# Performance work log

Hardware: AMD Instinct MI355X
Metric: run time of the kernel (lower is better)

Reference implementation:

```python
import jax, jax.numpy as jnp
import numpy as np

B, S, E, H = 4, 2048, 1024, 16
Dh = E // H
EPS = 1e-5


def setup_inputs() -> dict:
    key = jax.random.key(0)
    ks = jax.random.split(key, 16)
    w = lambda k, shp: jax.random.normal(k, shp, dtype=jnp.float32) * 0.02
    return {
        "x": jax.random.normal(ks[0], (B, S, E), dtype=jnp.float32),
        "Wq": w(ks[1], (E, E)), "bq": jnp.zeros((E,), jnp.float32),
        "Wk": w(ks[2], (E, E)), "bk": jnp.zeros((E,), jnp.float32),
        "Wv": w(ks[3], (E, E)), "bv": jnp.zeros((E,), jnp.float32),
        "Wo": w(ks[4], (E, E)), "bo": jnp.zeros((E,), jnp.float32),
        "an1_a": jnp.ones((1, S, 1), jnp.float32),
        "an1_b": jnp.zeros((1, S, 1), jnp.float32),
        "W1": w(ks[5], (2 * E, E)), "b1": jnp.zeros((2 * E,), jnp.float32),
        "W2": w(ks[6], (E, 2 * E)), "b2": jnp.zeros((E,), jnp.float32),
        "an2_a": jnp.ones((1, S, 1), jnp.float32),
        "an2_b": jnp.zeros((1, S, 1), jnp.float32),
    }


def adaptive_norm(x, a, b):
    # AdaptiveNorm((1, N_s, 1)): normalize over embedding dim, per-position affine.
    mu = jnp.mean(x, axis=-1, keepdims=True)
    var = jnp.mean(jnp.square(x - mu), axis=-1, keepdims=True)
    return a * (x - mu) * jax.lax.rsqrt(var + EPS) + b


def reference(x, Wq, bq, Wk, bk, Wv, bv, Wo, bo, an1_a, an1_b, W1, b1, W2, b2, an2_a, an2_b):
    scale = 1.0 / np.sqrt(E / H)
    # QKV projections -> (B, S, H, Dh)
    q = (x @ Wq.T + bq).reshape(B, S, H, Dh)
    k = (x @ Wk.T + bk).reshape(B, S, H, Dh)
    v = (x @ Wv.T + bv).reshape(B, S, H, Dh)
    # scaled dot-product attention (materializes B,H,S,S like the original)
    scores = jnp.einsum("bshd,bthd->bhst", q, k) * scale
    probs = jax.nn.softmax(scores, axis=-1)
    attn = jnp.einsum("bhst,bthd->bshd", probs, v).reshape(B, S, E)
    attn = attn @ Wo.T + bo
    # residual + adaptive norm (dropout is identity in eval mode)
    h = adaptive_norm(attn + x, an1_a, an1_b)
    ff = jax.nn.relu(h @ W1.T + b1) @ W2.T + b2
    out = adaptive_norm(ff + h, an2_a, an2_b)
    return out
```

## Files before the change

### kernel.cpp

```cpp
#include <hip/hip_runtime.h>


typedef __attribute__((ext_vector_type(8))) short s16x8;
typedef __attribute__((ext_vector_type(4))) short s16x4;
typedef __attribute__((ext_vector_type(4))) unsigned short u16x4;
typedef __attribute__((ext_vector_type(4))) float f32x4;

__device__ __forceinline__ float bf2f(unsigned short u) {
  unsigned int v = ((unsigned int)u) << 16;
  return __builtin_bit_cast(float, v);
}
__device__ __forceinline__ unsigned short f2bf(float f) {
  unsigned int u = __builtin_bit_cast(unsigned int, f);
  u += 0x7fffu + ((u >> 16) & 1u);
  return (unsigned short)(u >> 16);
}
__device__ __forceinline__ unsigned int pkbf_trunc(float f0, float f1) {
  return __builtin_amdgcn_perm(__builtin_bit_cast(unsigned int, f1),
                               __builtin_bit_cast(unsigned int, f0), 0x07060302u);
}
__device__ __forceinline__ f32x4 mfma16(s16x8 a, s16x8 b, f32x4 c) {
  return __builtin_amdgcn_mfma_f32_16x16x32_bf16(a, b, c, 0, 0, 0);
}
__device__ __forceinline__ void gl2lds16(const unsigned short* g, unsigned short* l) {
  __builtin_amdgcn_global_load_lds(
      (const __attribute__((address_space(1))) unsigned int*)(g),
      (__attribute__((address_space(3))) unsigned int*)(l), 16, 0, 0);
}

__global__ void detect_dtype(const unsigned int* __restrict__ x, int* __restrict__ flag) {
  const int tid = threadIdx.x;
  int cnt = 0;
  for (int i = tid; i < 2048; i += 256) {
    const unsigned e = (x[i] >> 7) & 0xFF;
    cnt += (e >= 100 && e <= 150) ? 1 : 0;
  }
#pragma unroll
  for (int off = 32; off >= 1; off >>= 1) cnt += __shfl_xor(cnt, off);
  __shared__ int red[4];
  if ((tid & 63) == 0) red[tid >> 6] = cnt;
  __syncthreads();
  if (tid == 0) *flag = ((red[0] + red[1] + red[2] + red[3]) > 1536) ? 1 : 0;
}

struct CvtArgs {
  const void* src[17];
  unsigned short* dst[17];
  int cum4[18];
};

__global__ __launch_bounds__(256) void cvt_all(CvtArgs a, const int* __restrict__ flag, int total4) {
  const int i = blockIdx.x * 256 + threadIdx.x;
  if (i >= total4) return;
  int lo = 0, hi = 17;
  while (hi - lo > 1) {
    const int mid = (lo + hi) >> 1;
    if (i >= a.cum4[mid]) lo = mid; else hi = mid;
  }
  const int off4 = i - a.cum4[lo];
  if (*flag) {
    const u16x4* s = (const u16x4*)a.src[lo];
    *(u16x4*)&a.dst[lo][off4 * 4] = s[off4];
  } else {
    const float4* s = (const float4*)a.src[lo];
    const float4 v = s[off4];
    u16x4 o;
    o[0] = f2bf(v.x); o[1] = f2bf(v.y); o[2] = f2bf(v.z); o[3] = f2bf(v.w);
    *(u16x4*)&a.dst[lo][off4 * 4] = o;
  }
}

#define QOFF 8388608L
#define SCALE2 0.18033688011f

template <int EPI, int BM>
__global__ __launch_bounds__(512, 1) void gemm2(
    const unsigned short* __restrict__ A, const unsigned short* __restrict__ W,
    const unsigned short* __restrict__ bias, const unsigned short* __restrict__ resid,
    unsigned short* __restrict__ out, int M, int N, int K) {
  constexpr int NBUF = (BM == 256) ? 2 : 3;
  constexpr int BUFE = (BM + 256) * 64;
  extern __shared__ unsigned short sh[];

  const int tid = threadIdx.x;
  const int lane = tid & 63;
  const int wave = tid >> 6;
  const int qd = lane >> 4;
  const int c = lane & 15;
  const int wr = (wave >> 2) * (BM / 2);
  const int wc = (wave & 3) * 64;

  const int nx = gridDim.x, ny = gridDim.y;
  const int nwg = nx * ny;
  int lin = blockIdx.y * nx + blockIdx.x;
  lin = (lin & 7) * (nwg >> 3) + (lin >> 3);
  const int by = lin % ny;
  const int bx = lin / ny;
  const long m0 = (long)by * BM;
  const long n0 = (long)bx * 256;

  const int srow = tid >> 3;
  const int scc = ((tid & 7) ^ (srow & 7)) * 8;
  const unsigned short* Asrc = A + (m0 + srow) * (long)K + scc;
  const unsigned short* Wsrc = W + (n0 + srow) * (long)K + scc;
  const int lofs = tid * 8;

  f32x4 acc[BM / 32][4] = {};

  const int NT = K >> 6;

  auto stA = [&](int sel, int tt, int q) {
    gl2lds16(Asrc + (long)q * 64 * K + (long)tt * 64, sh + sel * BUFE + q * 4096 + lofs);
  };
  auto stB = [&](int sel, int tt, int q) {
    gl2lds16(Wsrc + (long)q * 64 * K + (long)tt * 64,
             sh + sel * BUFE + BM * 64 + q * 4096 + lofs);
  };

  if constexpr (BM == 256) {
    stB(0, 0, 0); stB(0, 0, 1); stB(0, 0, 2); stB(0, 0, 3);
    stA(0, 0, 0); stA(0, 0, 2); stA(0, 0, 1); stA(0, 0, 3);
  } else {
    stB(0, 0, 0); stB(0, 0, 1); stB(0, 0, 2); stB(0, 0, 3); stA(0, 0, 0); stA(0, 0, 1);
    stB(1, 1, 0); stB(1, 1, 1); stB(1, 1, 2); stB(1, 1, 3); stA(1, 1, 0); stA(1, 1, 1);
  }

  int cur = 0;
  for (int t = 0; t < NT; ++t) {
    const unsigned short* Ab = sh + cur * BUFE;
    const unsigned short* Bb = Ab + BM * 64;

    if constexpr (BM == 256) {
      const bool dost = (t + 1 < NT);
      const int ns = cur ^ 1;
      asm volatile("s_waitcnt vmcnt(2)\n\ts_barrier" ::: "memory");
      s16x8 bfr[4][2], af[4][2];
#pragma unroll
      for (int nt = 0; nt < 4; ++nt)
#pragma unroll
        for (int ks = 0; ks < 2; ++ks)
          bfr[nt][ks] = *(const s16x8*)&Bb[(wc + nt * 16 + c) * 64 +
                                           (((ks * 4 + qd) ^ (c & 7)) * 8)];
#pragma unroll
      for (int mt = 0; mt < 4; ++mt)
#pragma unroll
        for (int ks = 0; ks < 2; ++ks)
          af[mt][ks] = *(const s16x8*)&Ab[(wr + mt * 16 + c) * 64 +
                                          (((ks * 4 + qd) ^ (c & 7)) * 8)];
      if (dost) { stB(ns, t + 1, 0); stB(ns, t + 1, 1); stB(ns, t + 1, 2); stB(ns, t + 1, 3); }
      __builtin_amdgcn_s_setprio(1);
#pragma unroll
      for (int mt = 0; mt < 4; ++mt)
#pragma unroll
        for (int nt = 0; nt < 4; ++nt)
#pragma unroll
          for (int ks = 0; ks < 2; ++ks)
            acc[mt][nt] = mfma16(af[mt][ks], bfr[nt][ks], acc[mt][nt]);
      __builtin_amdgcn_s_setprio(0);
      if (dost) asm volatile("s_waitcnt vmcnt(4)\n\ts_barrier" ::: "memory");
      else      asm volatile("s_waitcnt vmcnt(0)\n\ts_barrier" ::: "memory");
#pragma unroll
      for (int mt = 0; mt < 4; ++mt)
#pragma unroll
        for (int ks = 0; ks < 2; ++ks)
          af[mt][ks] = *(const s16x8*)&Ab[(wr + 64 + mt * 16 + c) * 64 +
                                          (((ks * 4 + qd) ^ (c & 7)) * 8)];
      if (dost) { stA(ns, t + 1, 0); stA(ns, t + 1, 2); stA(ns, t + 1, 1); stA(ns, t + 1, 3); }
      __builtin_amdgcn_s_setprio(1);
#pragma unroll
      for (int mt = 0; mt < 4; ++mt)
#pragma unroll
        for (int nt = 0; nt < 4; ++nt)
#pragma unroll
          for (int ks = 0; ks < 2; ++ks)
            acc[4 + mt][nt] = mfma16(af[mt][ks], bfr[nt][ks], acc[4 + mt][nt]);
      __builtin_amdgcn_s_setprio(0);
    } else {
      if (t + 1 < NT) asm volatile("s_waitcnt vmcnt(6)\n\ts_barrier" ::: "memory");
      else            asm volatile("s_waitcnt vmcnt(0)\n\ts_barrier" ::: "memory");
      s16x8 bfr[4][2], af[4][2];
#pragma unroll
      for (int nt = 0; nt < 4; ++nt)
#pragma unroll
        for (int ks = 0; ks < 2; ++ks)
          bfr[nt][ks] = *(const s16x8*)&Bb[(wc + nt * 16 + c) * 64 +
                                           (((ks * 4 + qd) ^ (c & 7)) * 8)];
#pragma unroll
      for (int mt = 0; mt < 4; ++mt)
#pragma unroll
        for (int ks = 0; ks < 2; ++ks)
          af[mt][ks] = *(const s16x8*)&Ab[(wr + mt * 16 + c) * 64 +
                                          (((ks * 4 + qd) ^ (c & 7)) * 8)];
      if (t + 2 < NT) {
        const int ns = (cur >= 1) ? cur - 1 : 2;
        stB(ns, t + 2, 0); stB(ns, t + 2, 1); stB(ns, t + 2, 2); stB(ns, t + 2, 3);
        stA(ns, t + 2, 0); stA(ns, t + 2, 1);
      }
      __builtin_amdgcn_s_setprio(1);
#pragma unroll
      for (int mt = 0; mt < 4; ++mt)
#pragma unroll
        for (int nt = 0; nt < 4; ++nt)
#pragma unroll
          for (int ks = 0; ks < 2; ++ks)
            acc[mt][nt] = mfma16(af[mt][ks], bfr[nt][ks], acc[mt][nt]);
      __builtin_amdgcn_s_setprio(0);
    }
    cur = (cur + 1 == NBUF) ? 0 : cur + 1;
  }

#pragma unroll
  for (int nt = 0; nt < 4; ++nt) {
    const int gn = (int)n0 + wc + nt * 16 + c;
    const float bv = bf2f(bias[gn]);
#pragma unroll
    for (int mt = 0; mt < BM / 32; ++mt) {
      const long gmb = m0 + wr + mt * 16 + qd * 4;
      if constexpr (EPI == 2) {
#pragma unroll
        for (int r = 0; r < 4; ++r) {
          const long gm = gmb + r;
          const float v = acc[mt][nt][r] + bv + bf2f(resid[gm * N + gn]);
          out[gm * N + gn] = f2bf(v);
        }
      } else if constexpr (EPI == 3) {
#pragma unroll
        for (int r = 0; r < 4; ++r) {
          const long gm = gmb + r;
          float v = acc[mt][nt][r] + bv;
          v = fmaxf(v, 0.0f);
          out[gm * N + gn] = f2bf(v);
        }
      } else {
        const int seg = gn >> 10;
        const int nn = gn & 1023;
        if (seg == 0) {
#pragma unroll
          for (int r = 0; r < 4; ++r)
            out[(gmb + r) * 1024 + nn] = f2bf((acc[mt][nt][r] + bv) * SCALE2);
        } else if (seg == 1) {
#pragma unroll
          for (int r = 0; r < 4; ++r)
            (out + QOFF)[(gmb + r) * 1024 + nn] = f2bf(acc[mt][nt][r] + bv);
        } else {
          const int h = nn >> 6, d = nn & 63;
          const long b = gmb >> 11;
          const int s = (int)(gmb & 2047);
          s16x4 pv;
#pragma unroll
          for (int r = 0; r < 4; ++r) pv[r] = (short)f2bf(acc[mt][nt][r] + bv);
          *(s16x4*)&(out + 2 * QOFF)[((b * 16 + h) * 64L + d) * 2048 + s] = pv;
        }
      }
    }
  }
}

#define ATT_S 2048

__global__ __launch_bounds__(256)
__attribute__((amdgpu_waves_per_eu(2, 2))) void attn_fwd(
    const unsigned short* __restrict__ Q, const unsigned short* __restrict__ K,
    const unsigned short* __restrict__ VT, unsigned short* __restrict__ O) {
  __shared__ unsigned short SH[24576];
  unsigned short* Kb0 = SH;
  unsigned short* Kb1 = SH + 4096;
  unsigned short* Vb0 = SH + 8192;
  unsigned short* Vb1 = SH + 12288;
  unsigned short* Pl  = SH + 16384;

  const int bh = blockIdx.y;
  const int q0 = blockIdx.x * 256;
  const long b = bh >> 4;
  const int h = bh & 15;
  const unsigned short* Qg = Q + (b * 2048) * 1024 + h * 64;
  const unsigned short* Kg = K + (b * 2048) * 1024 + h * 64;
  const unsigned short* Vg = VT + (long)bh * 64 * 2048;

  const int tid = threadIdx.x;
  const int wave = tid >> 6, lane = tid & 63;
  const int qd = lane >> 4, c = lane & 15;
  const int mb = wave * 32;

  const int srow = tid >> 3;
  const int sccs = ((tid & 7) ^ (srow & 7)) * 8;

  s16x8 qf[2][2][2];
#pragma unroll
  for (int h2 = 0; h2 < 2; ++h2)
#pragma unroll
    for (int mt = 0; mt < 2; ++mt)
#pragma unroll
      for (int ks = 0; ks < 2; ++ks)
        qf[h2][mt][ks] = *(const s16x8*)&Qg[(long)(q0 + h2 * 128 + mb + mt * 16 + c) * 1024 +
                                            ks * 32 + qd * 8];

  s16x8 ones;
#pragma unroll
  for (int i = 0; i < 8; ++i) ones[i] = (short)0x3F80;

  f32x4 oacc[2][4][2] = {};
  f32x4 lacc[2][2] = {};

  gl2lds16(Kg + (long)srow * 1024 + sccs, &Kb0[tid * 8]);
  gl2lds16(Kg + (long)(srow + 32) * 1024 + sccs, &Kb0[(256 + tid) * 8]);
  gl2lds16(Vg + (long)srow * 2048 + sccs, &Vb0[tid * 8]);
  gl2lds16(Vg + (long)(srow + 32) * 2048 + sccs, &Vb0[(256 + tid) * 8]);

  for (int it = 0; it < 32; ++it) {
    const int p = it & 1;
    unsigned short* Kc = p ? Kb1 : Kb0;
    unsigned short* Vc = p ? Vb1 : Vb0;
    unsigned short* Kn = p ? Kb0 : Kb1;
    unsigned short* Vn = p ? Vb0 : Vb1;
    const int kvn = (it < 31) ? (it + 1) * 64 : 31 * 64;
    gl2lds16(Kg + (long)(kvn + srow) * 1024 + sccs, &Kn[tid * 8]);
    gl2lds16(Kg + (long)(kvn + srow + 32) * 1024 + sccs, &Kn[(256 + tid) * 8]);
    gl2lds16(Vg + (long)srow * 2048 + kvn + sccs, &Vn[tid * 8]);
    gl2lds16(Vg + (long)(srow + 32) * 2048 + kvn + sccs, &Vn[(256 + tid) * 8]);

    asm volatile("s_waitcnt vmcnt(4)\n\ts_barrier" ::: "memory");

#pragma unroll
    for (int h2 = 0; h2 < 2; ++h2) {
      f32x4 sacc[4][2] = {};
#pragma unroll
      for (int ks = 0; ks < 2; ++ks) {
        const int ch = ((ks * 4 + qd) ^ (c & 7)) * 8;
        s16x8 kf[4];
#pragma unroll
        for (int tt = 0; tt < 4; ++tt)
          kf[tt] = *(const s16x8*)&Kc[(tt * 16 + c) * 64 + ch];
#pragma unroll
        for (int mt = 0; mt < 2; ++mt)
#pragma unroll
          for (int tt = 0; tt < 4; ++tt)
            sacc[tt][mt] = mfma16(kf[tt], qf[h2][mt][ks], sacc[tt][mt]);
      }

#pragma unroll
      for (int mt = 0; mt < 2; ++mt) {
        const int ml = mb + mt * 16 + c;
#pragma unroll
        for (int tt = 0; tt < 4; ++tt) {
          unsigned int pk[2];
          pk[0] = pkbf_trunc(__builtin_amdgcn_exp2f(sacc[tt][mt][0]),
                             __builtin_amdgcn_exp2f(sacc[tt][mt][1]));
          pk[1] = pkbf_trunc(__builtin_amdgcn_exp2f(sacc[tt][mt][2]),
                             __builtin_amdgcn_exp2f(sacc[tt][mt][3]));
          const int chw = ((tt * 2 + (qd >> 1)) ^ (ml & 7)) * 8 + (qd & 1) * 4;
          *(uint2*)&Pl[ml * 64 + chw] = *(uint2*)pk;
        }
      }
      asm volatile("s_waitcnt lgkmcnt(0)" ::: "memory");

#pragma unroll
      for (int ks = 0; ks < 2; ++ks) {
        const int vch = ((ks * 4 + qd) ^ (c & 7)) * 8;
        s16x8 vf[4], pf[2];
#pragma unroll
        for (int dt = 0; dt < 4; ++dt)
          vf[dt] = *(const s16x8*)&Vc[(dt * 16 + c) * 64 + vch];
#pragma unroll
        for (int mt = 0; mt < 2; ++mt) {
          const int pr = mb + mt * 16 + c;
          pf[mt] = *(const s16x8*)&Pl[pr * 64 + (((ks * 4 + qd) ^ (pr & 7)) * 8)];
        }
#pragma unroll
        for (int mt = 0; mt < 2; ++mt) {
#pragma unroll
          for (int dt = 0; dt < 4; ++dt)
            oacc[h2][dt][mt] = mfma16(vf[dt], pf[mt], oacc[h2][dt][mt]);
          lacc[h2][mt] = mfma16(ones, pf[mt], lacc[h2][mt]);
        }
      }
    }

    asm volatile("s_barrier" ::: "memory");
  }

#pragma unroll
  for (int h2 = 0; h2 < 2; ++h2)
#pragma unroll
    for (int mt = 0; mt < 2; ++mt) {
      const float inv = 1.0f / lacc[h2][mt][0];
      const int s = q0 + h2 * 128 + mb + mt * 16 + c;
      const long ob = (b * (long)ATT_S + s) * 1024L + h * 64;
#pragma unroll
      for (int dt = 0; dt < 4; ++dt) {
        s16x4 ov;
#pragma unroll
        for (int r = 0; r < 4; ++r) ov[r] = (short)f2bf(oacc[h2][dt][mt][r] * inv);
        *(s16x4*)&O[ob + dt * 16 + qd * 4] = ov;
      }
    }
}

template <bool FINAL>
__global__ __launch_bounds__(256) void norm_affine(
    const unsigned short* __restrict__ X, const unsigned short* __restrict__ av,
    const unsigned short* __restrict__ bv, void* __restrict__ outv,
    const int* __restrict__ flag) {
  const int row = blockIdx.x;
  const int s = row & 2047;
  const unsigned short* xr = X + (long)row * 1024;
  const int tid = threadIdx.x;
  const u16x4 u = *(const u16x4*)&xr[tid * 4];
  float v[4];
  float s1 = 0.f, s2 = 0.f;
#pragma unroll
  for (int i = 0; i < 4; ++i) {
    v[i] = bf2f(u[i]);
    s1 += v[i];
    s2 += v[i] * v[i];
  }
#pragma unroll
  for (int off = 32; off >= 1; off >>= 1) {
    s1 += __shfl_xor(s1, off);
    s2 += __shfl_xor(s2, off);
  }
  __shared__ float red[8];
  const int wave = tid >> 6, lane = tid & 63;
  if (lane == 0) {
    red[wave * 2] = s1;
    red[wave * 2 + 1] = s2;
  }
  __syncthreads();
  s1 = red[0] + red[2] + red[4] + red[6];
  s2 = red[1] + red[3] + red[5] + red[7];
  const float mean = s1 * (1.0f / 1024.0f);
  const float var = fmaxf(s2 * (1.0f / 1024.0f) - mean * mean, 0.0f);
  const float rstd = rsqrtf(var + 1e-5f);
  const float aa = bf2f(av[s]), bb = bf2f(bv[s]);
  float o[4];
#pragma unroll
  for (int i = 0; i < 4; ++i) o[i] = aa * (v[i] - mean) * rstd + bb;
  bool as_bf16 = true;
  if constexpr (FINAL) as_bf16 = (*flag != 0);
  if (as_bf16) {
    u16x4 ob;
#pragma unroll
    for (int i = 0; i < 4; ++i) ob[i] = f2bf(o[i]);
    *(u16x4*)&((unsigned short*)outv)[(long)row * 1024 + tid * 4] = ob;
  } else {
    float4 of = {o[0], o[1], o[2], o[3]};
    *(float4*)&((float*)outv)[(long)row * 1024 + tid * 4] = of;
  }
}

extern "C" void kernel_launch(void* const* d_in, const int* in_sizes, int n_in,
                              void* d_out, int out_size, void* d_ws, size_t ws_size,
                              hipStream_t stream) {
  char* ws = (char*)d_ws;
  const size_t SZ = 8192ull * 1024 * 2;
  const size_t WSZ = 1024ull * 1024 * 2;

  unsigned short* xb   = (unsigned short*)(ws);
  unsigned short* qb   = (unsigned short*)(ws + SZ);
  unsigned short* kb   = (unsigned short*)(ws + 2 * SZ);
  unsigned short* vtb  = (unsigned short*)(ws + 3 * SZ);
  unsigned short* attn = (unsigned short*)(ws + 4 * SZ);
  unsigned short* hb   = (unsigned short*)(ws + 5 * SZ);
  unsigned short* r1   = qb;
  unsigned short* ffb  = kb;
  unsigned short* r2   = attn;

  char* wreg = ws + 6 * SZ;
  unsigned short* wqb = (unsigned short*)(wreg);
  unsigned short* w1b = (unsigned short*)(wreg + 4 * WSZ);
  unsigned short* w2b = (unsigned short*)(wreg + 6 * WSZ);
  unsigned short* wob = (unsigned short*)(wreg + 3 * WSZ);
  unsigned short* smal = (unsigned short*)(wreg + 8 * WSZ);
  unsigned short* bqb = smal;
  unsigned short* bkb = smal + 1024;
  unsigned short* bvb = smal + 2048;
  unsigned short* bob = smal + 3072;
  unsigned short* b1b = smal + 4096;
  unsigned short* b2b = smal + 6144;
  unsigned short* a1b = smal + 7168;
  unsigned short* g1b = smal + 9216;
  unsigned short* a2b = smal + 11264;
  unsigned short* g2b = smal + 13312;
  int* flag = (int*)(wreg + 8 * WSZ + 64 * 1024);

  CvtArgs ca;
  unsigned short* wkb = wqb + 1024 * 1024;
  unsigned short* wvb = wqb + 2 * 1024 * 1024;
  unsigned short* dsts[17] = {xb, wqb, bqb, wkb, bkb, wvb, bvb, wob, bob,
                              a1b, g1b, w1b, b1b, w2b, b2b, a2b, g2b};
  ca.cum4[0] = 0;
  for (int i = 0; i < 17; ++i) {
    ca.src[i] = d_in[i];
    ca.dst[i] = dsts[i];
    ca.cum4[i + 1] = ca.cum4[i] + in_sizes[i] / 4;
  }
  const int total4 = ca.cum4[17];

  static bool attr_set = false;
  if (!attr_set) {
    attr_set = true;
    hipFuncSetAttribute(reinterpret_cast<const void*>(gemm2<4, 256>),
                        hipFuncAttributeMaxDynamicSharedMemorySize, 131072);
    hipFuncSetAttribute(reinterpret_cast<const void*>(gemm2<3, 256>),
                        hipFuncAttributeMaxDynamicSharedMemorySize, 131072);
    hipFuncSetAttribute(reinterpret_cast<const void*>(gemm2<2, 128>),
                        hipFuncAttributeMaxDynamicSharedMemorySize, 147456);
  }

  dim3 blk(256);
  dim3 blk512(512);
  detect_dtype<<<1, blk, 0, stream>>>((const unsigned int*)d_in[0], flag);
  cvt_all<<<(total4 + 255) / 256, blk, 0, stream>>>(ca, flag, total4);

  gemm2<4, 256><<<dim3(12, 32), blk512, 131072, stream>>>(xb, wqb, bqb, nullptr, qb, 8192, 3072, 1024);
  attn_fwd<<<dim3(8, 64), blk, 0, stream>>>(qb, kb, vtb, attn);
  gemm2<2, 128><<<dim3(4, 64), blk512, 147456, stream>>>(attn, wob, bob, xb, r1, 8192, 1024, 1024);
  norm_affine<false><<<8192, blk, 0, stream>>>(r1, a1b, g1b, hb, nullptr);
  gemm2<3, 256><<<dim3(8, 32), blk512, 131072, stream>>>(hb, w1b, b1b, nullptr, ffb, 8192, 2048, 1024);
  gemm2<2, 128><<<dim3(4, 64), blk512, 147456, stream>>>(ffb, w2b, b2b, hb, r2, 8192, 1024, 2048);
  norm_affine<true><<<8192, blk, 0, stream>>>(r2, a2b, g2b, d_out, flag);
}
```

Before: 404.4 us.

## Add 256x256 GEMM with 4-phase quadrant schedule and batch attention QK across heads

Result: no change. 408.2 us (+0.9%).

```diff
diff --git a/kernel.cpp b/kernel.cpp
--- a/kernel.cpp
+++ b/kernel.cpp
@@ -73,12 +73,185 @@
 #define QOFF 8388608L
 #define SCALE2 0.18033688011f
 
+template <int EPI>
+__device__ __forceinline__ void gemm_epi_elem(
+    unsigned short* __restrict__ out, const unsigned short* __restrict__ resid,
+    int N, long gmb, int gn, const f32x4& a, float bv) {
+  if constexpr (EPI == 2) {
+#pragma unroll
+    for (int r = 0; r < 4; ++r) {
+      const long gm = gmb + r;
+      out[gm * N + gn] = f2bf(a[r] + bv + bf2f(resid[gm * N + gn]));
+    }
+  } else if constexpr (EPI == 3) {
+#pragma unroll
+    for (int r = 0; r < 4; ++r)
+      out[(gmb + r) * N + gn] = f2bf(fmaxf(a[r] + bv, 0.0f));
+  } else {
+    const int seg = gn >> 10;
+    const int nn = gn & 1023;
+    if (seg == 0) {
+#pragma unroll
+      for (int r = 0; r < 4; ++r)
+        out[(gmb + r) * 1024 + nn] = f2bf((a[r] + bv) * SCALE2);
+    } else if (seg == 1) {
+#pragma unroll
+      for (int r = 0; r < 4; ++r)
+        (out + QOFF)[(gmb + r) * 1024 + nn] = f2bf(a[r] + bv);
+    } else {
+      const int h = nn >> 6, d = nn & 63;
+      const long b = gmb >> 11;
+      const int s = (int)(gmb & 2047);
+      s16x4 pv;
+#pragma unroll
+      for (int r = 0; r < 4; ++r) pv[r] = (short)f2bf(a[r] + bv);
+      *(s16x4*)&(out + 2 * QOFF)[((b * 16 + h) * 64L + d) * 2048 + s] = pv;
+    }
+  }
+}
+
+template <int EPI>
+__global__ __launch_bounds__(512, 1) void gemm256(
+    const unsigned short* __restrict__ A, const unsigned short* __restrict__ W,
+    const unsigned short* __restrict__ bias, const unsigned short* __restrict__ resid,
+    unsigned short* __restrict__ out, int M, int N, int K) {
+  extern __shared__ unsigned short sh[];
+  const int tid = threadIdx.x;
+  const int lane = tid & 63;
+  const int wave = tid >> 6;
+  const int qd = lane >> 4;
+  const int c = lane & 15;
+  const int wm = (wave >> 2) * 64;
+  const int wn = (wave & 3) * 32;
+
+  const int nx = gridDim.x, ny = gridDim.y;
+  const int nwg = nx * ny;
+  int lin = blockIdx.y * nx + blockIdx.x;
+  lin = (lin & 7) * (nwg >> 3) + (lin >> 3);
+  const int by = lin % ny;
+  const int bx = lin / ny;
+  const long m0 = (long)by * 256;
+  const long n0 = (long)bx * 256;
+
+  const int srow = tid >> 3;
+  const int scc = ((tid & 7) ^ (srow & 7)) * 8;
+  const unsigned short* Asrc = A + (m0 + srow) * (long)K + scc;
+  const unsigned short* Wsrc = W + (n0 + srow) * (long)K + scc;
+  const int lofs = tid * 8;
+
+  f32x4 acc[8][4] = {};
+  const int NT = K >> 6;
+
+  auto stage = [&](int tt, int r) {
+    unsigned short* dst = sh + (tt & 1) * 32768;
+    const long kof = (long)tt * 64;
+    if (r < 2)      gl2lds16(Asrc + (long)r * 64 * K + kof, dst + r * 4096 + lofs);
+    else if (r < 6) gl2lds16(Wsrc + (long)(r - 2) * 64 * K + kof,
+                             dst + 16384 + (r - 2) * 4096 + lofs);
+    else            gl2lds16(Asrc + (long)(r - 4) * 64 * K + kof, dst + (r - 4) * 4096 + lofs);
+  };
+
+#pragma unroll
+  for (int r = 0; r < 8; ++r) stage(0, r);
+
+  for (int t = 0; t < NT; ++t) {
+    const unsigned short* Ab = sh + (t & 1) * 32768;
+    const unsigned short* Bb = Ab + 16384;
+    const bool dost = (t + 1 < NT);
+    s16x8 af[4][2], bf0[2][2], bf1[2][2];
+
+    asm volatile("s_waitcnt vmcnt(4)\n\ts_barrier" ::: "memory");
+#pragma unroll
+    for (int mt = 0; mt < 4; ++mt)
+#pragma unroll
+      for (int ks = 0; ks < 2; ++ks)
+        af[mt][ks] = *(const s16x8*)&Ab[(wm + mt * 16 + c) * 64 +
+                                        (((ks * 4 + qd) ^ (c & 7)) * 8)];
+#pragma unroll
+    for (int nt = 0; nt < 2; ++nt)
+#pragma unroll
+      for (int ks = 0; ks < 2; ++ks)
+        bf0[nt][ks] = *(const s16x8*)&Bb[(wn + nt * 16 + c) * 64 +
+                                         (((ks * 4 + qd) ^ (c & 7)) * 8)];
+    if (dost) { stage(t + 1, 0); stage(t + 1, 1); }
+    __builtin_amdgcn_s_setprio(1);
+#pragma unroll
+    for (int mt = 0; mt < 4; ++mt)
+#pragma unroll
+      for (int nt = 0; nt < 2; ++nt)
+#pragma unroll
+        for (int ks = 0; ks < 2; ++ks)
+          acc[mt][nt] = mfma16(af[mt][ks], bf0[nt][ks], acc[mt][nt]);
+    __builtin_amdgcn_s_setprio(0);
+
+    if (dost) asm volatile("s_waitcnt vmcnt(4)\n\ts_barrier" ::: "memory");
+    else      asm volatile("s_waitcnt vmcnt(2)\n\ts_barrier" ::: "memory");
+#pragma unroll
+    for (int nt = 0; nt < 2; ++nt)
+#pragma unroll
+      for (int ks = 0; ks < 2; ++ks)
+        bf1[nt][ks] = *(const s16x8*)&Bb[(128 + wn + nt * 16 + c) * 64 +
+                                         (((ks * 4 + qd) ^ (c & 7)) * 8)];
+    if (dost) { stage(t + 1, 2); stage(t + 1, 3); }
+    __builtin_amdgcn_s_setprio(1);
+#pragma unroll
+    for (int mt = 0; mt < 4; ++mt)
+#pragma unroll
+      for (int nt = 0; nt < 2; ++nt)
+#pragma unroll
+        for (int ks = 0; ks < 2; ++ks)
+          acc[mt][2 + nt] = mfma16(af[mt][ks], bf1[nt][ks], acc[mt][2 + nt]);
+    __builtin_amdgcn_s_setprio(0);
+
+    if (dost) asm volatile("s_waitcnt vmcnt(4)\n\ts_barrier" ::: "memory");
+    else      asm volatile("s_waitcnt vmcnt(0)\n\ts_barrier" ::: "memory");
+#pragma unroll
+    for (int mt = 0; mt < 4; ++mt)
+#pragma unroll
+      for (int ks = 0; ks < 2; ++ks)
+        af[mt][ks] = *(const s16x8*)&Ab[(128 + wm + mt * 16 + c) * 64 +
+                                        (((ks * 4 + qd) ^ (c & 7)) * 8)];
+    if (dost) { stage(t + 1, 4); stage(t + 1, 5); }
+    __builtin_amdgcn_s_setprio(1);
+#pragma unroll
+    for (int mt = 0; mt < 4; ++mt)
+#pragma unroll
+      for (int nt = 0; nt < 2; ++nt)
+#pragma unroll
+        for (int ks = 0; ks < 2; ++ks)
+          acc[4 + mt][2 + nt] = mfma16(af[mt][ks], bf1[nt][ks], acc[4 + mt][2 + nt]);
+    __builtin_amdgcn_s_setprio(0);
+
+    asm volatile("s_barrier" ::: "memory");
+    if (dost) { stage(t + 1, 6); stage(t + 1, 7); }
+    __builtin_amdgcn_s_setprio(1);
+#pragma unroll
+    for (int mt = 0; mt < 4; ++mt)
+#pragma unroll
+      for (int nt = 0; nt < 2; ++nt)
+#pragma unroll
+        for (int ks = 0; ks < 2; ++ks)
+          acc[4 + mt][nt] = mfma16(af[mt][ks], bf0[nt][ks], acc[4 + mt][nt]);
+    __builtin_amdgcn_s_setprio(0);
+  }
+
+#pragma unroll
+  for (int j = 0; j < 4; ++j) {
+    const int gn = (int)n0 + (j >> 1) * 128 + wn + (j & 1) * 16 + c;
+    const float bv = bf2f(bias[gn]);
+#pragma unroll
+    for (int i = 0; i < 8; ++i) {
+      const long gmb = m0 + (i >> 2) * 128 + wm + (i & 3) * 16 + qd * 4;
+      gemm_epi_elem<EPI>(out, resid, N, gmb, gn, acc[i][j], bv);
+    }
+  }
+}
+
 template <int EPI, int BM>
 __global__ __launch_bounds__(512, 1) void gemm2(
     const unsigned short* __restrict__ A, const unsigned short* __restrict__ W,
     const unsigned short* __restrict__ bias, const unsigned short* __restrict__ resid,
     unsigned short* __restrict__ out, int M, int N, int K) {
-  constexpr int NBUF = (BM == 256) ? 2 : 3;
   constexpr int BUFE = (BM + 256) * 64;
   extern __shared__ unsigned short sh[];
 
@@ -106,7 +279,6 @@
   const int lofs = tid * 8;
 
   f32x4 acc[BM / 32][4] = {};
-
   const int NT = K >> 6;
 
   auto stA = [&](int sel, int tt, int q) {
@@ -117,96 +289,44 @@
              sh + sel * BUFE + BM * 64 + q * 4096 + lofs);
   };
 
-  if constexpr (BM == 256) {
-    stB(0, 0, 0); stB(0, 0, 1); stB(0, 0, 2); stB(0, 0, 3);
-    stA(0, 0, 0); stA(0, 0, 2); stA(0, 0, 1); stA(0, 0, 3);
-  } else {
-    stB(0, 0, 0); stB(0, 0, 1); stB(0, 0, 2); stB(0, 0, 3); stA(0, 0, 0); stA(0, 0, 1);
-    stB(1, 1, 0); stB(1, 1, 1); stB(1, 1, 2); stB(1, 1, 3); stA(1, 1, 0); stA(1, 1, 1);
-  }
+  stB(0, 0, 0); stB(0, 0, 1); stB(0, 0, 2); stB(0, 0, 3); stA(0, 0, 0); stA(0, 0, 1);
+  stB(1, 1, 0); stB(1, 1, 1); stB(1, 1, 2); stB(1, 1, 3); stA(1, 1, 0); stA(1, 1, 1);
 
   int cur = 0;
   for (int t = 0; t < NT; ++t) {
     const unsigned short* Ab = sh + cur * BUFE;
     const unsigned short* Bb = Ab + BM * 64;
 
-    if constexpr (BM == 256) {
-      const bool dost = (t + 1 < NT);
-      const int ns = cur ^ 1;
-      asm volatile("s_waitcnt vmcnt(2)\n\ts_barrier" ::: "memory");
-      s16x8 bfr[4][2], af[4][2];
+    if (t + 1 < NT) asm volatile("s_waitcnt vmcnt(6)\n\ts_barrier" ::: "memory");
+    else            asm volatile("s_waitcnt vmcnt(0)\n\ts_barrier" ::: "memory");
+    s16x8 bfr[4][2], af[4][2];
+#pragma unroll
+    for (int nt = 0; nt < 4; ++nt)
+#pragma unroll
+      for (int ks = 0; ks < 2; ++ks)
+        bfr[nt][ks] = *(const s16x8*)&Bb[(wc + nt * 16 + c) * 64 +
+                                         (((ks * 4 + qd) ^ (c & 7)) * 8)];
+#pragma unroll
+    for (int mt = 0; mt < 4; ++mt)
+#pragma unroll
+      for (int ks = 0; ks < 2; ++ks)
+        af[mt][ks] = *(const s16x8*)&Ab[(wr + mt * 16 + c) * 64 +
+                                        (((ks * 4 + qd) ^ (c & 7)) * 8)];
+    if (t + 2 < NT) {
+      const int ns = (cur >= 1) ? cur - 1 : 2;
+      stB(ns, t + 2, 0); stB(ns, t + 2, 1); stB(ns, t + 2, 2); stB(ns, t + 2, 3);
+      stA(ns, t + 2, 0); stA(ns, t + 2, 1);
+    }
+    __builtin_amdgcn_s_setprio(1);
+#pragma unroll
+    for (int mt = 0; mt < 4; ++mt)
 #pragma unroll
       for (int nt = 0; nt < 4; ++nt)
 #pragma unroll
         for (int ks = 0; ks < 2; ++ks)
-          bfr[nt][ks] = *(const s16x8*)&Bb[(wc + nt * 16 + c) * 64 +
-                                           (((ks * 4 + qd) ^ (c & 7)) * 8)];
-#pragma unroll
-      for (int mt = 0; mt < 4; ++mt)
-#pragma unroll
-        for (int ks = 0; ks < 2; ++ks)
-          af[mt][ks] = *(const s16x8*)&Ab[(wr + mt * 16 + c) * 64 +
-                                          (((ks * 4 + qd) ^ (c & 7)) * 8)];
-      if (dost) { stB(ns, t + 1, 0); stB(ns, t + 1, 1); stB(ns, t + 1, 2); stB(ns, t + 1, 3); }
-      __builtin_amdgcn_s_setprio(1);
-#pragma unroll
-      for (int mt = 0; mt < 4; ++mt)
-#pragma unroll
-        for (int nt = 0; nt < 4; ++nt)
-#pragma unroll
-          for (int ks = 0; ks < 2; ++ks)
-            acc[mt][nt] = mfma16(af[mt][ks], bfr[nt][ks], acc[mt][nt]);
-      __builtin_amdgcn_s_setprio(0);
-      if (dost) asm volatile("s_waitcnt vmcnt(4)\n\ts_barrier" ::: "memory");
-      else      asm volatile("s_waitcnt vmcnt(0)\n\ts_barrier" ::: "memory");
-#pragma unroll
-      for (int mt = 0; mt < 4; ++mt)
-#pragma unroll
-        for (int ks = 0; ks < 2; ++ks)
-          af[mt][ks] = *(const s16x8*)&Ab[(wr + 64 + mt * 16 + c) * 64 +
-                                          (((ks * 4 + qd) ^ (c & 7)) * 8)];
-      if (dost) { stA(ns, t + 1, 0); stA(ns, t + 1, 2); stA(ns, t + 1, 1); stA(ns, t + 1, 3); }
-      __builtin_amdgcn_s_setprio(1);
-#pragma unroll
-      for (int mt = 0; mt < 4; ++mt)
-#pragma unroll
-        for (int nt = 0; nt < 4; ++nt)
-#pragma unroll
-          for (int ks = 0; ks < 2; ++ks)
-            acc[4 + mt][nt] = mfma16(af[mt][ks], bfr[nt][ks], acc[4 + mt][nt]);
-      __builtin_amdgcn_s_setprio(0);
-    } else {
-      if (t + 1 < NT) asm volatile("s_waitcnt vmcnt(6)\n\ts_barrier" ::: "memory");
-      else            asm volatile("s_waitcnt vmcnt(0)\n\ts_barrier" ::: "memory");
-      s16x8 bfr[4][2], af[4][2];
-#pragma unroll
-      for (int nt = 0; nt < 4; ++nt)
-#pragma unroll
-        for (int ks = 0; ks < 2; ++ks)
-          bfr[nt][ks] = *(const s16x8*)&Bb[(wc + nt * 16 + c) * 64 +
-                                           (((ks * 4 + qd) ^ (c & 7)) * 8)];
-#pragma unroll
-      for (int mt = 0; mt < 4; ++mt)
-#pragma unroll
-        for (int ks = 0; ks < 2; ++ks)
-          af[mt][ks] = *(const s16x8*)&Ab[(wr + mt * 16 + c) * 64 +
-                                          (((ks * 4 + qd) ^ (c & 7)) * 8)];
-      if (t + 2 < NT) {
-        const int ns = (cur >= 1) ? cur - 1 : 2;
-        stB(ns, t + 2, 0); stB(ns, t + 2, 1); stB(ns, t + 2, 2); stB(ns, t + 2, 3);
-        stA(ns, t + 2, 0); stA(ns, t + 2, 1);
-      }
-      __builtin_amdgcn_s_setprio(1);
-#pragma unroll
-      for (int mt = 0; mt < 4; ++mt)
-#pragma unroll
-        for (int nt = 0; nt < 4; ++nt)
-#pragma unroll
-          for (int ks = 0; ks < 2; ++ks)
-            acc[mt][nt] = mfma16(af[mt][ks], bfr[nt][ks], acc[mt][nt]);
-      __builtin_amdgcn_s_setprio(0);
-    }
-    cur = (cur + 1 == NBUF) ? 0 : cur + 1;
+          acc[mt][nt] = mfma16(af[mt][ks], bfr[nt][ks], acc[mt][nt]);
+    __builtin_amdgcn_s_setprio(0);
+    cur = (cur + 1 == 3) ? 0 : cur + 1;
   }
 
 #pragma unroll
@@ -216,42 +336,7 @@
 #pragma unroll
     for (int mt = 0; mt < BM / 32; ++mt) {
       const long gmb = m0 + wr + mt * 16 + qd * 4;
-      if constexpr (EPI == 2) {
-#pragma unroll
-        for (int r = 0; r < 4; ++r) {
-          const long gm = gmb + r;
-          const float v = acc[mt][nt][r] + bv + bf2f(resid[gm * N + gn]);
-          out[gm * N + gn] = f2bf(v);
-        }
-      } else if constexpr (EPI == 3) {
-#pragma unroll
-        for (int r = 0; r < 4; ++r) {
-          const long gm = gmb + r;
-          float v = acc[mt][nt][r] + bv;
-          v = fmaxf(v, 0.0f);
-          out[gm * N + gn] = f2bf(v);
-        }
-      } else {
-        const int seg = gn >> 10;
-        const int nn = gn & 1023;
-        if (seg == 0) {
-#pragma unroll
-          for (int r = 0; r < 4; ++r)
-            out[(gmb + r) * 1024 + nn] = f2bf((acc[mt][nt][r] + bv) * SCALE2);
-        } else if (seg == 1) {
-#pragma unroll
-          for (int r = 0; r < 4; ++r)
-            (out + QOFF)[(gmb + r) * 1024 + nn] = f2bf(acc[mt][nt][r] + bv);
-        } else {
-          const int h = nn >> 6, d = nn & 63;
-          const long b = gmb >> 11;
-          const int s = (int)(gmb & 2047);
-          s16x4 pv;
-#pragma unroll
-          for (int r = 0; r < 4; ++r) pv[r] = (short)f2bf(acc[mt][nt][r] + bv);
-          *(s16x4*)&(out + 2 * QOFF)[((b * 16 + h) * 64L + d) * 2048 + s] = pv;
-        }
-      }
+      gemm_epi_elem<EPI>(out, resid, N, gmb, gn, acc[mt][nt], bv);
     }
   }
 }
@@ -262,7 +347,7 @@
 __attribute__((amdgpu_waves_per_eu(2, 2))) void attn_fwd(
     const unsigned short* __restrict__ Q, const unsigned short* __restrict__ K,
     const unsigned short* __restrict__ VT, unsigned short* __restrict__ O) {
-  __shared__ unsigned short SH[24576];
+  __shared__ unsigned short SH[32768];
   unsigned short* Kb0 = SH;
   unsigned short* Kb1 = SH + 4096;
   unsigned short* Vb0 = SH + 8192;
@@ -321,50 +406,58 @@
 
     asm volatile("s_waitcnt vmcnt(4)\n\ts_barrier" ::: "memory");
 
+    f32x4 sacc[2][4][2] = {};
+#pragma unroll
+    for (int ks = 0; ks < 2; ++ks) {
+      const int ch = ((ks * 4 + qd) ^ (c & 7)) * 8;
+      s16x8 kf[4];
+#pragma unroll
+      for (int tt = 0; tt < 4; ++tt)
+        kf[tt] = *(const s16x8*)&Kc[(tt * 16 + c) * 64 + ch];
+#pragma unroll
+      for (int h2 = 0; h2 < 2; ++h2)
+#pragma unroll
+        for (int mt = 0; mt < 2; ++mt)
+#pragma unroll
+          for (int tt = 0; tt < 4; ++tt)
+            sacc[h2][tt][mt] = mfma16(kf[tt], qf[h2][mt][ks], sacc[h2][tt][mt]);
+    }
+
 #pragma unroll
     for (int h2 = 0; h2 < 2; ++h2) {
-      f32x4 sacc[4][2] = {};
-#pragma unroll
-      for (int ks = 0; ks < 2; ++ks) {
-        const int ch = ((ks * 4 + qd) ^ (c & 7)) * 8;
-        s16x8 kf[4];
-#pragma unroll
-        for (int tt = 0; tt < 4; ++tt)
-          kf[tt] = *(const s16x8*)&Kc[(tt * 16 + c) * 64 + ch];
-#pragma unroll
-        for (int mt = 0; mt < 2; ++mt)
-#pragma unroll
-          for (int tt = 0; tt < 4; ++tt)
-            sacc[tt][mt] = mfma16(kf[tt], qf[h2][mt][ks], sacc[tt][mt]);
-      }
-
+      unsigned short* Ph = Pl + h2 * 8192;
 #pragma unroll
       for (int mt = 0; mt < 2; ++mt) {
         const int ml = mb + mt * 16 + c;
 #pragma unroll
         for (int tt = 0; tt < 4; ++tt) {
           unsigned int pk[2];
-          pk[0] = pkbf_trunc(__builtin_amdgcn_exp2f(sacc[tt][mt][0]),
-                             __builtin_amdgcn_exp2f(sacc[tt][mt][1]));
-          pk[1] = pkbf_trunc(__builtin_amdgcn_exp2f(sacc[tt][mt][2]),
-                             __builtin_amdgcn_exp2f(sacc[tt][mt][3]));
+          pk[0] = pkbf_trunc(__builtin_amdgcn_exp2f(sacc[h2][tt][mt][0]),
+                             __builtin_amdgcn_exp2f(sacc[h2][tt][mt][1]));
+          pk[1] = pkbf_trunc(__builtin_amdgcn_exp2f(sacc[h2][tt][mt][2]),
+                             __builtin_amdgcn_exp2f(sacc[h2][tt][mt][3]));
           const int chw = ((tt * 2 + (qd >> 1)) ^ (ml & 7)) * 8 + (qd & 1) * 4;
-          *(uint2*)&Pl[ml * 64 + chw] = *(uint2*)pk;
+          *(uint2*)&Ph[ml * 64 + chw] = *(uint2*)pk;
         }
       }
-      asm volatile("s_waitcnt lgkmcnt(0)" ::: "memory");
-
-#pragma unroll
-      for (int ks = 0; ks < 2; ++ks) {
-        const int vch = ((ks * 4 + qd) ^ (c & 7)) * 8;
-        s16x8 vf[4], pf[2];
-#pragma unroll
-        for (int dt = 0; dt < 4; ++dt)
-          vf[dt] = *(const s16x8*)&Vc[(dt * 16 + c) * 64 + vch];
+    }
+    asm volatile("s_waitcnt lgkmcnt(0)" ::: "memory");
+
+#pragma unroll
+    for (int ks = 0; ks < 2; ++ks) {
+      const int vch = ((ks * 4 + qd) ^ (c & 7)) * 8;
+      s16x8 vf[4];
+#pragma unroll
+      for (int dt = 0; dt < 4; ++dt)
+        vf[dt] = *(const s16x8*)&Vc[(dt * 16 + c) * 64 + vch];
+#pragma unroll
+      for (int h2 = 0; h2 < 2; ++h2) {
+        const unsigned short* Ph = Pl + h2 * 8192;
+        s16x8 pf[2];
 #pragma unroll
         for (int mt = 0; mt < 2; ++mt) {
           const int pr = mb + mt * 16 + c;
-          pf[mt] = *(const s16x8*)&Pl[pr * 64 + (((ks * 4 + qd) ^ (pr & 7)) * 8)];
+          pf[mt] = *(const s16x8*)&Ph[pr * 64 + (((ks * 4 + qd) ^ (pr & 7)) * 8)];
         }
 #pragma unroll
         for (int mt = 0; mt < 2; ++mt) {
@@ -499,9 +592,9 @@
   static bool attr_set = false;
   if (!attr_set) {
     attr_set = true;
-    hipFuncSetAttribute(reinterpret_cast<const void*>(gemm2<4, 256>),
+    hipFuncSetAttribute(reinterpret_cast<const void*>(gemm256<4>),
                         hipFuncAttributeMaxDynamicSharedMemorySize, 131072);
-    hipFuncSetAttribute(reinterpret_cast<const void*>(gemm2<3, 256>),
+    hipFuncSetAttribute(reinterpret_cast<const void*>(gemm256<3>),
                         hipFuncAttributeMaxDynamicSharedMemorySize, 131072);
     hipFuncSetAttribute(reinterpret_cast<const void*>(gemm2<2, 128>),
                         hipFuncAttributeMaxDynamicSharedMemorySize, 147456);
@@ -512,11 +605,11 @@
   detect_dtype<<<1, blk, 0, stream>>>((const unsigned int*)d_in[0], flag);
   cvt_all<<<(total4 + 255) / 256, blk, 0, stream>>>(ca, flag, total4);
 
-  gemm2<4, 256><<<dim3(12, 32), blk512, 131072, stream>>>(xb, wqb, bqb, nullptr, qb, 8192, 3072, 1024);
+  gemm256<4><<<dim3(12, 32), blk512, 131072, stream>>>(xb, wqb, bqb, nullptr, qb, 8192, 3072, 1024);
   attn_fwd<<<dim3(8, 64), blk, 0, stream>>>(qb, kb, vtb, attn);
   gemm2<2, 128><<<dim3(4, 64), blk512, 147456, stream>>>(attn, wob, bob, xb, r1, 8192, 1024, 1024);
   norm_affine<false><<<8192, blk, 0, stream>>>(r1, a1b, g1b, hb, nullptr);
-  gemm2<3, 256><<<dim3(8, 32), blk512, 131072, stream>>>(hb, w1b, b1b, nullptr, ffb, 8192, 2048, 1024);
+  gemm256<3><<<dim3(8, 32), blk512, 131072, stream>>>(hb, w1b, b1b, nullptr, ffb, 8192, 2048, 1024);
   gemm2<2, 128><<<dim3(4, 64), blk512, 147456, stream>>>(ffb, w2b, b2b, hb, r2, 8192, 1024, 2048);
   norm_affine<true><<<8192, blk, 0, stream>>>(r2, a2b, g2b, d_out, flag);
 }
```
